# Optimization experiments

Hardware: AMD Instinct MI355X
Metric: run time of the kernel (lower is better)

The kernel has to match this reference:

```python
import jax, jax.numpy as jnp
import numpy as np

B, T, C, H = 8, 2048, 1024, 16
N_LAYER, LAYER_ID = 12, 1
NH = C // H           # head size = 64
CHUNK = 256


def setup_inputs() -> dict:
    key = jax.random.key(0)
    ks = jax.random.split(key, 10)
    # deterministic init matching the torch __init__
    ratio_0_to_1 = LAYER_ID / (N_LAYER - 1)
    ratio_1_to_almost0 = 1.0 - LAYER_ID / N_LAYER
    ddd = np.arange(C, dtype=np.float32) / C
    time_maa_k = (1.0 - ddd ** ratio_1_to_almost0).astype(np.float32)
    time_maa_v = (1.0 - (ddd ** ratio_1_to_almost0 + 0.3 * ratio_0_to_1)).astype(np.float32)
    time_maa_r = (1.0 - ddd ** (0.5 * ratio_1_to_almost0)).astype(np.float32)
    h_idx = np.arange(H, dtype=np.float32)
    time_decay = (-6.0 + 5.0 * (h_idx / (H - 1)) ** (0.7 + 1.3 * ratio_0_to_1)).astype(np.float32)
    s = 0.02
    return {
        "x": jax.random.normal(ks[0], (B, T, C), jnp.float32),
        "volatility": jax.random.uniform(ks[1], (B, T), jnp.float32),
        "Wvol": jax.random.normal(ks[2], (C, 1), jnp.float32) * s,
        "bvol": jnp.zeros((C,), jnp.float32),
        "time_maa_k": jnp.asarray(time_maa_k),
        "time_maa_v": jnp.asarray(time_maa_v),
        "time_maa_r": jnp.asarray(time_maa_r),
        "time_decay": jnp.asarray(time_decay),
        "Wk": jax.random.normal(ks[3], (C, C), jnp.float32) * s,
        "Wv": jax.random.normal(ks[4], (C, C), jnp.float32) * s,
        "Wr": jax.random.normal(ks[5], (C, C), jnp.float32) * s,
        "Wo": jax.random.normal(ks[6], (C, C), jnp.float32) * s,
        "gn_w": 1.0 + jax.random.normal(ks[7], (C,), jnp.float32) * s,
        "gn_b": jax.random.normal(ks[8], (C,), jnp.float32) * s,
    }


def reference(x, volatility, Wvol, bvol, time_maa_k, time_maa_v, time_maa_r,
              time_decay, Wk, Wv, Wr, Wo, gn_w, gn_b):
    b, t, c = x.shape
    h = time_decay.shape[0]
    n = c // h
    nc = t // CHUNK

    # volatility gating: sigmoid(Linear(1->C))
    v_emb = jax.nn.sigmoid(volatility[:, :, None] * Wvol[:, 0] + bvol)  # (B,T,C)
    x = x * v_emb

    # time shift (zero-pad one step at the front, drop last)
    xx = jnp.pad(x, ((0, 0), (1, 0), (0, 0)))[:, :-1] - x
    xk = x + xx * time_maa_k
    xv = x + xx * time_maa_v
    xr = x + xx * time_maa_r

    r = (xr @ Wr.T).reshape(b, t, h, n).transpose(0, 2, 1, 3)  # (B,H,T,N)
    k = (xk @ Wk.T).reshape(b, t, h, n).transpose(0, 2, 1, 3)
    v = (xv @ Wv.T).reshape(b, t, h, n).transpose(0, 2, 1, 3)

    w = jnp.exp(-jnp.exp(time_decay))[None, :, None, None]  # scalar decay per head

    # chunked linear-attention recurrence (faithful to torch loop, chunk=256, no intra-chunk mask)
    rc = r.reshape(b, h, nc, CHUNK, n).transpose(2, 0, 1, 3, 4)  # (nc,B,H,CK,N)
    kc = k.reshape(b, h, nc, CHUNK, n).transpose(2, 0, 1, 3, 4)
    vc = v.reshape(b, h, nc, CHUNK, n).transpose(2, 0, 1, 3, 4)

    def step(state, rkv):
        rr, kk, vv = rkv  # each (B,H,CK,N)
        att = jnp.einsum('bhtn,bhsn->bhts', rr, kk)            # r @ k^T
        y = w * (jnp.einsum('bhts,bhsn->bhtn', att, vv)
                 + jnp.einsum('bhtn,bhnm->bhtm', rr, state))
        new_state = w * (state + jnp.einsum('bhsn,bhsm->bhnm', kk, vv))
        return new_state, y

    state0 = jnp.zeros((b, h, n, n), x.dtype)
    _, ys = jax.lax.scan(step, state0, (rc, kc, vc))            # (nc,B,H,CK,N)
    y = ys.transpose(1, 2, 0, 3, 4).reshape(b, h, t, n)
    y = y.transpose(0, 2, 1, 3).reshape(b * t, c)

    # GroupNorm with H groups over channels
    yg = y.reshape(b * t, h, n)
    mu = yg.mean(-1, keepdims=True)
    var = yg.var(-1, keepdims=True)
    yg = (yg - mu) * jax.lax.rsqrt(var + 1e-5)
    y = (yg.reshape(b * t, c) * gn_w + gn_b).reshape(b, t, c)

    return y @ Wo.T  # dropout is identity in eval
```

## Files before the change

### kernel.cpp

```cpp
#include <hip/hip_runtime.h>

typedef unsigned short u16;
typedef __attribute__((ext_vector_type(4))) unsigned int u32x4;
typedef __attribute__((ext_vector_type(4))) float f32x4;
typedef __attribute__((ext_vector_type(8))) short s16x8;

#define B_ 8
#define T_ 2048
#define C_ 1024
#define H_ 16
#define HS_ 64
#define CHUNK_ 256
#define NC_ 8

union U8 { u32x4 u; u16 h[8]; };

__device__ __forceinline__ float b2f(u16 v) {
    union { unsigned int i; float f; } c; c.i = ((unsigned int)v) << 16; return c.f;
}
__device__ __forceinline__ u16 f2b(float f) {
    union { float f; unsigned int i; } c; c.f = f;
    unsigned int i = c.i;
    return (u16)((i + 0x7FFFu + ((i >> 16) & 1u)) >> 16);
}
__device__ __forceinline__ float fsig(float z) {
    return __builtin_amdgcn_rcpf(1.f + __expf(-z));
}

typedef __attribute__((address_space(1))) void GV;
typedef __attribute__((address_space(3))) void LV;
__device__ __forceinline__ void glds16(const void* g, void* l) {
    __builtin_amdgcn_global_load_lds((GV*)g, (LV*)l, 16, 0, 0);
}

__global__ __launch_bounds__(256) void cvt4_kernel(
    const float* __restrict__ s0, const float* __restrict__ s1,
    const float* __restrict__ s2, const float* __restrict__ s3,
    u16* __restrict__ dst)
{
    int i = blockIdx.x * 256 + threadIdx.x;
    int m = i >> 17;
    const float* s = (m == 0) ? s0 : (m == 1) ? s1 : (m == 2) ? s2 : s3;
    size_t j = (size_t)(i & 131071) * 8;
    f32x4 a = *reinterpret_cast<const f32x4*>(s + j);
    f32x4 b = *reinterpret_cast<const f32x4*>(s + j + 4);
    U8 o;
    #pragma unroll
    for (int k = 0; k < 4; k++) { o.h[k] = f2b(a[k]); o.h[4 + k] = f2b(b[k]); }
    *reinterpret_cast<u32x4*>(dst + (size_t)m * C_ * C_ + j) = o.u;
}

__global__ __launch_bounds__(256) void mix_kernel(
    const float* __restrict__ x, const float* __restrict__ vol,
    const float* __restrict__ Wvol, const float* __restrict__ bvol,
    const float* __restrict__ mk, const float* __restrict__ mv, const float* __restrict__ mr,
    u16* __restrict__ xk, u16* __restrict__ xv, u16* __restrict__ xr)
{
    int idx = blockIdx.x * 256 + threadIdx.x;
    int c0 = (idx & 127) * 8;
    int bt8 = idx >> 7;
    int t0  = (bt8 & 255) * 8;
    int b   = bt8 >> 8;
    size_t rowOff = ((size_t)b * T_ + t0) * C_ + c0;

    float wv[8], bv[8], mkv[8], mvv[8], mrv[8];
    #pragma unroll
    for (int j = 0; j < 8; j += 4) {
        f32x4 a;
        a = *reinterpret_cast<const f32x4*>(Wvol + c0 + j);
        wv[j] = a[0]; wv[j+1] = a[1]; wv[j+2] = a[2]; wv[j+3] = a[3];
        a = *reinterpret_cast<const f32x4*>(bvol + c0 + j);
        bv[j] = a[0]; bv[j+1] = a[1]; bv[j+2] = a[2]; bv[j+3] = a[3];
        a = *reinterpret_cast<const f32x4*>(mk + c0 + j);
        mkv[j] = a[0]; mkv[j+1] = a[1]; mkv[j+2] = a[2]; mkv[j+3] = a[3];
        a = *reinterpret_cast<const f32x4*>(mv + c0 + j);
        mvv[j] = a[0]; mvv[j+1] = a[1]; mvv[j+2] = a[2]; mvv[j+3] = a[3];
        a = *reinterpret_cast<const f32x4*>(mr + c0 + j);
        mrv[j] = a[0]; mrv[j+1] = a[1]; mrv[j+2] = a[2]; mrv[j+3] = a[3];
    }

    const float* volb = vol + (size_t)b * T_;
    float gp[8];
    if (t0 == 0) {
        #pragma unroll
        for (int j = 0; j < 8; j++) gp[j] = 0.f;
    } else {
        float vp = volb[t0 - 1];
        #pragma unroll
        for (int j = 0; j < 8; j += 4) {
            f32x4 a = *reinterpret_cast<const f32x4*>(x + rowOff - C_ + j);
            gp[j]   = a[0] * fsig(vp * wv[j]   + bv[j]);
            gp[j+1] = a[1] * fsig(vp * wv[j+1] + bv[j+1]);
            gp[j+2] = a[2] * fsig(vp * wv[j+2] + bv[j+2]);
            gp[j+3] = a[3] * fsig(vp * wv[j+3] + bv[j+3]);
        }
    }

    #pragma unroll
    for (int s = 0; s < 8; s++) {
        float vc = volb[t0 + s];
        size_t off = rowOff + (size_t)s * C_;
        float g[8];
        #pragma unroll
        for (int j = 0; j < 8; j += 4) {
            f32x4 a = *reinterpret_cast<const f32x4*>(x + off + j);
            g[j]   = a[0] * fsig(vc * wv[j]   + bv[j]);
            g[j+1] = a[1] * fsig(vc * wv[j+1] + bv[j+1]);
            g[j+2] = a[2] * fsig(vc * wv[j+2] + bv[j+2]);
            g[j+3] = a[3] * fsig(vc * wv[j+3] + bv[j+3]);
        }
        U8 ok, ov, orr;
        #pragma unroll
        for (int j = 0; j < 8; j++) {
            float xx = gp[j] - g[j];
            ok.h[j]  = f2b(g[j] + xx * mkv[j]);
            ov.h[j]  = f2b(g[j] + xx * mvv[j]);
            orr.h[j] = f2b(g[j] + xx * mrv[j]);
            gp[j] = g[j];
        }
        *reinterpret_cast<u32x4*>(xk + off) = ok.u;
        *reinterpret_cast<u32x4*>(xv + off) = ov.u;
        *reinterpret_cast<u32x4*>(xr + off) = orr.u;
    }
}

#define GBM_ 256
#define GBN_ 256
#define GBK_ 64
#define GK_  1024
#define GNT_ 16
#define GEMM_LDS_BYTES 131072

template<int MODE>
__global__ __launch_bounds__(512, 2) void gemm_bt(
    const u16* __restrict__ A, const u16* __restrict__ W, void* __restrict__ Cc)
{
    extern __shared__ __align__(16) u16 lds[];
    const int tid  = threadIdx.x;
    const int lane = tid & 63, w = tid >> 6;
    const int r16  = lane & 15, quad = lane >> 4;
    const int wm2  = w >> 2;
    const int wn4  = w & 3;
    const int id   = blockIdx.x;
    const int bm   = id & 63, bn = id >> 6;

    const u16* Ab = A + (size_t)bm * GBM_ * GK_;
    const u16* Wb = W + (size_t)bn * GBN_ * GK_;

    const int srow8  = lane >> 3;
    const int schunk = ((lane & 7) ^ srow8) * 8;
    const u16* aSrc = Ab + (size_t)(w * 16 + srow8) * GK_ + schunk;
    const u16* bSrc = Wb + (size_t)(w * 16 + srow8) * GK_ + schunk;

    const int fA0 = (wm2 * 128 + r16) * 64;
    const int fB0 = 16384 + (wn4 * 64 + r16) * 64;
    const int c0 = ((quad)     ^ (r16 & 7)) * 8;
    const int c1 = ((quad | 4) ^ (r16 & 7)) * 8;

    f32x4 acc[8][4];
    #pragma unroll
    for (int mi = 0; mi < 8; mi++)
        #pragma unroll
        for (int ni = 0; ni < 4; ni++)
            acc[mi][ni] = f32x4{0.f, 0.f, 0.f, 0.f};

#define STQ(tt, h) do {                                                       \
    const size_t ko_ = (size_t)(tt) * 64;                                     \
    u16* db_ = lds + (((tt) & 1) * 32768) + ((h) * 128 + w * 16) * 64;        \
    glds16(aSrc + (size_t)((h) * 128)     * GK_ + ko_, db_);                  \
    glds16(aSrc + (size_t)((h) * 128 + 8) * GK_ + ko_, db_ + 512);            \
    glds16(bSrc + (size_t)((h) * 128)     * GK_ + ko_, db_ + 16384);          \
    glds16(bSrc + (size_t)((h) * 128 + 8) * GK_ + ko_, db_ + 16384 + 512);    \
} while (0)

#define PH_BAR() do { asm volatile("" ::: "memory");                          \
    __builtin_amdgcn_s_barrier(); asm volatile("" ::: "memory"); } while (0)
#define PH_LGKM0() do { asm volatile("s_waitcnt lgkmcnt(0)" ::: "memory");    \
    __builtin_amdgcn_sched_barrier(0); } while (0)
#define LDFA(CO) { _Pragma("unroll") for (int mi = 0; mi < 8; mi++)           \
    fa[mi] = *reinterpret_cast<const s16x8*>(lds + pb + fA0 + mi * 1024 + (CO)); }
#define LDFB(NH, CO) { _Pragma("unroll") for (int ni = 0; ni < 2; ni++)       \
    fb[ni] = *reinterpret_cast<const s16x8*>(lds + pb + fB0 + ((NH) * 2 + ni) * 1024 + (CO)); }
#define MFMA16(NH) do { __builtin_amdgcn_s_setprio(1);                        \
    _Pragma("unroll") for (int mi = 0; mi < 8; mi++) {                        \
        acc[mi][(NH)*2+0] = __builtin_amdgcn_mfma_f32_16x16x32_bf16(          \
            fa[mi], fb[0], acc[mi][(NH)*2+0], 0, 0, 0);                       \
        acc[mi][(NH)*2+1] = __builtin_amdgcn_mfma_f32_16x16x32_bf16(          \
            fa[mi], fb[1], acc[mi][(NH)*2+1], 0, 0, 0);                       \
    } __builtin_amdgcn_s_setprio(0); } while (0)

    STQ(0, 0);
    STQ(0, 1);
    asm volatile("s_waitcnt vmcnt(0)" ::: "memory");
    PH_BAR();

    for (int t = 0; t < GNT_; ++t) {
        const int pb = (t & 1) * 32768;
        s16x8 fa[8], fb[2];
        LDFA(c0); LDFB(0, c0);
        if (t + 1 < GNT_) STQ(t + 1, 0);
        PH_BAR(); PH_LGKM0(); MFMA16(0); PH_BAR();
        LDFB(1, c0);
        PH_BAR(); PH_LGKM0(); MFMA16(1); PH_BAR();
        LDFA(c1); LDFB(0, c1);
        if (t + 1 < GNT_) STQ(t + 1, 1);
        PH_BAR(); PH_LGKM0(); MFMA16(0); PH_BAR();
        LDFB(1, c1);
        PH_BAR(); PH_LGKM0(); MFMA16(1);
        asm volatile("s_waitcnt vmcnt(0)" ::: "memory");
        PH_BAR();
    }
#undef STQ
#undef LDFA
#undef LDFB
#undef MFMA16
#undef PH_LGKM0
#undef PH_BAR

    if constexpr (MODE == 0) {
        float* C = (float*)Cc;
        #pragma unroll
        for (int mi = 0; mi < 8; mi++) {
            int row0 = bm * GBM_ + wm2 * 128 + mi * 16 + quad * 4;
            #pragma unroll
            for (int ni = 0; ni < 4; ni++) {
                int col = bn * GBN_ + wn4 * 64 + ni * 16 + r16;
                #pragma unroll
                for (int i = 0; i < 4; i++)
                    C[(size_t)(row0 + i) * C_ + col] = acc[mi][ni][i];
            }
        }
    } else if constexpr (MODE == 1) {
        u16* ep = lds + w * 4608;
        u16* C = (u16*)Cc;
        #pragma unroll
        for (int half = 0; half < 2; half++) {
            #pragma unroll
            for (int mi2 = 0; mi2 < 4; mi2++) {
                int mi = half * 4 + mi2;
                #pragma unroll
                for (int ni = 0; ni < 4; ni++)
                    #pragma unroll
                    for (int i = 0; i < 4; i++)
                        ep[(mi2 * 16 + quad * 4 + i) * 72 + ni * 16 + r16] =
                            f2b(acc[mi][ni][i]);
            }
            asm volatile("s_waitcnt lgkmcnt(0)" ::: "memory");
            __builtin_amdgcn_sched_barrier(0);
            #pragma unroll
            for (int it = 0; it < 8; it++) {
                int rr = it * 8 + (lane >> 3);
                u32x4 val = *reinterpret_cast<const u32x4*>(ep + rr * 72 + (lane & 7) * 8);
                size_t grow = (size_t)(bm * GBM_ + wm2 * 128 + half * 64 + rr);
                *reinterpret_cast<u32x4*>(
                    C + grow * C_ + bn * GBN_ + wn4 * 64 + (lane & 7) * 8) = val;
            }
            asm volatile("s_waitcnt vmcnt(0) lgkmcnt(0)" ::: "memory");
        }
    } else {
        u16* ep = lds + w * 8192;
        #pragma unroll
        for (int mi = 0; mi < 8; mi++) {
            const int chunk = mi * 2 + (quad >> 1);
            const int rsub = (quad & 1) * 4;
            #pragma unroll
            for (int ni = 0; ni < 4; ni++) {
                const int col = ni * 16 + r16;
                u16* p = ep + col * 128 + ((chunk ^ col) & 15) * 8 + rsub;
                p[0] = f2b(acc[mi][ni][0]);
                p[1] = f2b(acc[mi][ni][1]);
                p[2] = f2b(acc[mi][ni][2]);
                p[3] = f2b(acc[mi][ni][3]);
            }
        }
        asm volatile("s_waitcnt lgkmcnt(0)" ::: "memory");
        __builtin_amdgcn_sched_barrier(0);
        u16* C = (u16*)Cc;
        const int cl = lane >> 2, ch4 = lane & 3;
        #pragma unroll
        for (int it = 0; it < 16; it++) {
            const int col_l = (it & 3) * 16 + cl;
            const int chunk = (it >> 2) * 4 + ch4;
            u32x4 val = *reinterpret_cast<const u32x4*>(
                ep + col_l * 128 + ((chunk ^ col_l) & 15) * 8);
            const size_t gcol = (size_t)(bn * GBN_ + wn4 * 64 + col_l);
            const size_t grow = (size_t)(bm * GBM_ + wm2 * 128 + chunk * 8);
            *reinterpret_cast<u32x4*>(C + gcol * 16384 + grow) = val;
        }
    }
}

__global__ __launch_bounds__(256) void kvscan_kernel(
    const u16* __restrict__ kT, const u16* __restrict__ vT,
    const float* __restrict__ td, u16* __restrict__ stT)
{
    const int bm2 = blockIdx.x;
    const int mh = bm2 & 1, bh = bm2 >> 1;
    const int h = bh & (H_ - 1), b = bh >> 4;
    const float wdec = expf(-expf(td[h]));
    const int tid = threadIdx.x, lane = tid & 63, wave = tid >> 6;
    const int r16 = lane & 15, quad = lane >> 4;
    const int n0 = wave * 16;

    const size_t tb = (size_t)b * T_ + quad * 8;
    const u16* vr  = vT + (size_t)(h * HS_ + n0 + r16) * 16384 + tb;
    const u16* kr0 = kT + (size_t)(h * HS_ + mh * 32 + r16) * 16384 + tb;
    const u16* kr1 = kr0 + (size_t)16 * 16384;

    f32x4 st[2];
    st[0] = f32x4{0.f, 0.f, 0.f, 0.f};
    st[1] = f32x4{0.f, 0.f, 0.f, 0.f};

    for (int j = 0; j < NC_; j++) {
        f32x4 acc[2];
        acc[0] = f32x4{0.f, 0.f, 0.f, 0.f};
        acc[1] = f32x4{0.f, 0.f, 0.f, 0.f};
        const int jb = j * CHUNK_;
        #pragma unroll
        for (int ks = 0; ks < 8; ks++) {
            const int co = jb + ks * 32;
            s16x8 fa  = *reinterpret_cast<const s16x8*>(vr  + co);
            s16x8 fb0 = *reinterpret_cast<const s16x8*>(kr0 + co);
            s16x8 fb1 = *reinterpret_cast<const s16x8*>(kr1 + co);
            acc[0] = __builtin_amdgcn_mfma_f32_16x16x32_bf16(fa, fb0, acc[0], 0, 0, 0);
            acc[1] = __builtin_amdgcn_mfma_f32_16x16x32_bf16(fa, fb1, acc[1], 0, 0, 0);
        }
        u16* out = stT + ((size_t)bh * NC_ + j) * 4096;
        #pragma unroll
        for (int mi = 0; mi < 2; mi++) {
            st[mi] = (st[mi] + acc[mi]) * wdec;
            #pragma unroll
            for (int i = 0; i < 4; i++)
                out[(n0 + quad * 4 + i) * HS_ + mh * 32 + mi * 16 + r16] =
                    f2b(st[mi][i]);
        }
    }
}

__global__ __launch_bounds__(256) void rstate_gn_kernel(
    const u16* __restrict__ r, const u16* __restrict__ stT,
    const float* __restrict__ gnw, const float* __restrict__ gnb, u16* __restrict__ ygn)
{
    int blk = blockIdx.x;
    int c  = blk & (NC_ - 1);
    int bh = blk >> 3;
    int h = bh & (H_ - 1);
    int b = bh >> 4;
    __shared__ __align__(16) u16 sT[HS_ * 72];
    int tid = threadIdx.x, lane = tid & 63, wave = tid >> 6;
    int r16 = lane & 15, quad = lane >> 4;

    const u16* sg = stT + (size_t)blk * (HS_ * HS_);
    for (int i = tid; i < 512; i += 256) {
        int n = i >> 3, c8 = (i & 7) * 8;
        *reinterpret_cast<u32x4*>(&sT[n * 72 + c8]) =
            *reinterpret_cast<const u32x4*>(sg + n * HS_ + c8);
    }
    __syncthreads();

    size_t rowBase = (size_t)(b * T_ + c * CHUNK_ + wave * 64);
    f32x4 acc[4][4];
    #pragma unroll
    for (int mi = 0; mi < 4; mi++)
        #pragma unroll
        for (int ni = 0; ni < 4; ni++)
            acc[mi][ni] = f32x4{0.f, 0.f, 0.f, 0.f};

    #pragma unroll
    for (int ks = 0; ks < 2; ks++) {
        int kb = ks * 32 + quad * 8;
        s16x8 fa[4], fb[4];
        #pragma unroll
        for (int mi = 0; mi < 4; mi++)
            fa[mi] = *reinterpret_cast<const s16x8*>(
                r + (rowBase + mi * 16 + r16) * C_ + h * HS_ + kb);
        #pragma unroll
        for (int ni = 0; ni < 4; ni++)
            fb[ni] = *reinterpret_cast<const s16x8*>(&sT[(ni * 16 + r16) * 72 + kb]);
        #pragma unroll
        for (int mi = 0; mi < 4; mi++)
            #pragma unroll
            for (int ni = 0; ni < 4; ni++)
                acc[mi][ni] = __builtin_amdgcn_mfma_f32_16x16x32_bf16(fa[mi], fb[ni], acc[mi][ni], 0, 0, 0);
    }

    float gwv[4], gbv[4];
    #pragma unroll
    for (int ni = 0; ni < 4; ni++) {
        int col = ni * 16 + r16;
        gwv[ni] = gnw[h * HS_ + col];
        gbv[ni] = gnb[h * HS_ + col];
    }
    #pragma unroll
    for (int mi = 0; mi < 4; mi++) {
        float s1[4], s2[4];
        #pragma unroll
        for (int i = 0; i < 4; i++) {
            float s = 0.f, ss = 0.f;
            #pragma unroll
            for (int ni = 0; ni < 4; ni++) {
                float v = acc[mi][ni][i];
                s += v; ss += v * v;
            }
            s1[i] = s; s2[i] = ss;
        }
        #pragma unroll
        for (int d = 1; d < 16; d <<= 1) {
            #pragma unroll
            for (int i = 0; i < 4; i++) {
                s1[i] += __shfl_xor(s1[i], d);
                s2[i] += __shfl_xor(s2[i], d);
            }
        }
        #pragma unroll
        for (int i = 0; i < 4; i++) {
            float mu = s1[i] * (1.f / 64.f);
            float var = s2[i] * (1.f / 64.f) - mu * mu;
            float sc = rsqrtf(var + 1e-5f);
            size_t ob = (rowBase + mi * 16 + quad * 4 + i) * C_ + h * HS_;
            #pragma unroll
            for (int ni = 0; ni < 4; ni++)
                ygn[ob + ni * 16 + r16] = f2b((acc[mi][ni][i] - mu) * sc * gwv[ni] + gbv[ni]);
        }
    }
}

extern "C" void kernel_launch(void* const* d_in, const int* in_sizes, int n_in,
                              void* d_out, int out_size, void* d_ws, size_t ws_size,
                              hipStream_t stream) {
    const float* x    = (const float*)d_in[0];
    const float* vol  = (const float*)d_in[1];
    const float* Wvol = (const float*)d_in[2];
    const float* bvol = (const float*)d_in[3];
    const float* mk   = (const float*)d_in[4];
    const float* mv   = (const float*)d_in[5];
    const float* mr   = (const float*)d_in[6];
    const float* td   = (const float*)d_in[7];
    const float* Wk   = (const float*)d_in[8];
    const float* Wv   = (const float*)d_in[9];
    const float* Wr   = (const float*)d_in[10];
    const float* Wo   = (const float*)d_in[11];
    const float* gnw  = (const float*)d_in[12];
    const float* gnb  = (const float*)d_in[13];
    float* out = (float*)d_out;

    static bool init_attr = []() {
        hipFuncSetAttribute(reinterpret_cast<const void*>(gemm_bt<0>),
                            hipFuncAttributeMaxDynamicSharedMemorySize, GEMM_LDS_BYTES);
        hipFuncSetAttribute(reinterpret_cast<const void*>(gemm_bt<1>),
                            hipFuncAttributeMaxDynamicSharedMemorySize, GEMM_LDS_BYTES);
        hipFuncSetAttribute(reinterpret_cast<const void*>(gemm_bt<2>),
                            hipFuncAttributeMaxDynamicSharedMemorySize, GEMM_LDS_BYTES);
        return true;
    }();
    (void)init_attr;

    char* ws = (char*)d_ws;
    const size_t SLOT = (size_t)B_ * T_ * C_ * 2;
    u16* xr = (u16*)(ws + 0 * SLOT);
    u16* xk = (u16*)(ws + 1 * SLOT);
    u16* xv = (u16*)(ws + 2 * SLOT);
    u16* rb = (u16*)(ws + 3 * SLOT);
    u16* kbT = (u16*)(ws + 0 * SLOT);
    u16* vbT = (u16*)(ws + 1 * SLOT);
    u16* stT = (u16*)(ws + 2 * SLOT + SLOT / 2);
    u16* ygn = (u16*)(ws + 0 * SLOT);
    u16* wtb = (u16*)(ws + 4 * SLOT);
    u16* wrb = wtb;
    u16* wkb = wrb + (size_t)C_ * C_;
    u16* wvb = wkb + (size_t)C_ * C_;
    u16* wob = wvb + (size_t)C_ * C_;

    cvt4_kernel<<<dim3(4 * (C_ * C_ / 8) / 256), dim3(256), 0, stream>>>(Wr, Wk, Wv, Wo, wtb);

    mix_kernel<<<dim3(1024), dim3(256), 0, stream>>>(
        x, vol, Wvol, bvol, mk, mv, mr, xk, xv, xr);

    gemm_bt<1><<<dim3(256), dim3(512), GEMM_LDS_BYTES, stream>>>(xr, wrb, rb);
    gemm_bt<2><<<dim3(256), dim3(512), GEMM_LDS_BYTES, stream>>>(xk, wkb, kbT);
    gemm_bt<2><<<dim3(256), dim3(512), GEMM_LDS_BYTES, stream>>>(xv, wvb, vbT);

    kvscan_kernel<<<dim3(B_ * H_ * 2), dim3(256), 0, stream>>>(kbT, vbT, td, stT);

    rstate_gn_kernel<<<dim3(B_ * H_ * NC_), dim3(256), 0, stream>>>(rb, stT, gnw, gnb, ygn);

    gemm_bt<0><<<dim3(256), dim3(512), GEMM_LDS_BYTES, stream>>>(ygn, wob, out);
}
```

Baseline: 339.4 us.

## Tile transposed K/V layout and stage kvscan loads through LDS with wider blocks

The MODE-2 GEMM epilogue now writes K^T/V^T in 16x32 tiles (16 channels by 32 timesteps, each tile contiguous) instead of plain row-major transposed rows. kvscan uses 512 threads and double-buffered global-to-LDS staging of those tiles, and each of its 8 waves computes one 16x16 state block. Separately, mix_kernel handles 4 timesteps per thread with twice as many blocks, and the GEMM issues both next-tile stage loads at the start of each iteration. The aim is coalesced, overlapped memory access in the scan and more parallelism, in exchange for 96KB of LDS per block and coupling the tiled layout between the two kernels.

```diff
diff --git a/kernel.cpp b/kernel.cpp
--- a/kernel.cpp
+++ b/kernel.cpp
@@ -58,9 +58,9 @@
 {
     int idx = blockIdx.x * 256 + threadIdx.x;
     int c0 = (idx & 127) * 8;
-    int bt8 = idx >> 7;
-    int t0  = (bt8 & 255) * 8;
-    int b   = bt8 >> 8;
+    int bt4 = idx >> 7;
+    int t0  = (bt4 & 511) * 4;
+    int b   = bt4 >> 9;
     size_t rowOff = ((size_t)b * T_ + t0) * C_ + c0;
 
     float wv[8], bv[8], mkv[8], mvv[8], mrv[8];
@@ -97,7 +97,7 @@
     }
 
     #pragma unroll
-    for (int s = 0; s < 8; s++) {
+    for (int s = 0; s < 4; s++) {
         float vc = volb[t0 + s];
         size_t off = rowOff + (size_t)s * C_;
         float g[8];
@@ -198,12 +198,11 @@
         const int pb = (t & 1) * 32768;
         s16x8 fa[8], fb[2];
         LDFA(c0); LDFB(0, c0);
-        if (t + 1 < GNT_) STQ(t + 1, 0);
+        if (t + 1 < GNT_) { STQ(t + 1, 0); STQ(t + 1, 1); }
         PH_BAR(); PH_LGKM0(); MFMA16(0); PH_BAR();
         LDFB(1, c0);
         PH_BAR(); PH_LGKM0(); MFMA16(1); PH_BAR();
         LDFA(c1); LDFB(0, c1);
-        if (t + 1 < GNT_) STQ(t + 1, 1);
         PH_BAR(); PH_LGKM0(); MFMA16(0); PH_BAR();
         LDFB(1, c1);
         PH_BAR(); PH_LGKM0(); MFMA16(1);
@@ -277,64 +276,79 @@
         __builtin_amdgcn_sched_barrier(0);
         u16* C = (u16*)Cc;
         const int cl = lane >> 2, ch4 = lane & 3;
+        const int gc0 = bn * 16 + wn4 * 4;
+        const int tt0 = bm * 8 + wm2 * 4;
         #pragma unroll
         for (int it = 0; it < 16; it++) {
             const int col_l = (it & 3) * 16 + cl;
             const int chunk = (it >> 2) * 4 + ch4;
             u32x4 val = *reinterpret_cast<const u32x4*>(
                 ep + col_l * 128 + ((chunk ^ col_l) & 15) * 8);
-            const size_t gcol = (size_t)(bn * GBN_ + wn4 * 64 + col_l);
-            const size_t grow = (size_t)(bm * GBM_ + wm2 * 128 + chunk * 8);
-            *reinterpret_cast<u32x4*>(C + gcol * 16384 + grow) = val;
-        }
-    }
-}
-
-__global__ __launch_bounds__(256) void kvscan_kernel(
+            const size_t tile = (size_t)(gc0 + (it & 3)) * 512 + tt0 + (it >> 2);
+            *reinterpret_cast<u32x4*>(C + tile * 512 + cl * 32 + ch4 * 8) = val;
+        }
+    }
+}
+
+#define KVS_LDS_BYTES 98304
+
+__global__ __launch_bounds__(512) void kvscan_kernel(
     const u16* __restrict__ kT, const u16* __restrict__ vT,
     const float* __restrict__ td, u16* __restrict__ stT)
 {
+    extern __shared__ __align__(16) u16 klds[];
     const int bm2 = blockIdx.x;
     const int mh = bm2 & 1, bh = bm2 >> 1;
     const int h = bh & (H_ - 1), b = bh >> 4;
     const float wdec = expf(-expf(td[h]));
-    const int tid = threadIdx.x, lane = tid & 63, wave = tid >> 6;
+    const int tid = threadIdx.x, lane = tid & 63, w = tid >> 6;
     const int r16 = lane & 15, quad = lane >> 4;
-    const int n0 = wave * 16;
-
-    const size_t tb = (size_t)b * T_ + quad * 8;
-    const u16* vr  = vT + (size_t)(h * HS_ + n0 + r16) * 16384 + tb;
-    const u16* kr0 = kT + (size_t)(h * HS_ + mh * 32 + r16) * 16384 + tb;
-    const u16* kr1 = kr0 + (size_t)16 * 16384;
-
-    f32x4 st[2];
-    st[0] = f32x4{0.f, 0.f, 0.f, 0.f};
-    st[1] = f32x4{0.f, 0.f, 0.f, 0.f};
-
-    for (int j = 0; j < NC_; j++) {
-        f32x4 acc[2];
-        acc[0] = f32x4{0.f, 0.f, 0.f, 0.f};
-        acc[1] = f32x4{0.f, 0.f, 0.f, 0.f};
-        const int jb = j * CHUNK_;
+    const int cgn = w >> 1;
+    const int ck  = w & 1;
+    const int tt0 = b * 64;
+    const int loff = r16 * 32 + quad * 8;
+
+#define KSTG(jj, bb) do {                                                     \
+    u16* db_ = klds + (bb) * 24576;                                           \
+    _Pragma("unroll")                                                         \
+    for (int q = 0; q < 6; q++) {                                             \
+        const int tau = w * 6 + q;                                            \
+        const u16* src;                                                       \
+        if (tau < 32)                                                         \
+            src = vT + ((size_t)(h * 4 + (tau >> 3)) * 512 +                  \
+                        tt0 + (jj) * 8 + (tau & 7)) * 512;                    \
+        else                                                                  \
+            src = kT + ((size_t)(h * 4 + mh * 2 + ((tau - 32) >> 3)) * 512 +  \
+                        tt0 + (jj) * 8 + ((tau - 32) & 7)) * 512;             \
+        glds16(src + (size_t)lane * 8, db_ + tau * 512);                      \
+    }                                                                         \
+} while (0)
+
+    KSTG(0, 0);
+
+    f32x4 st = f32x4{0.f, 0.f, 0.f, 0.f};
+    for (int j = 0; j < NC_; ++j) {
+        asm volatile("s_waitcnt vmcnt(0)" ::: "memory");
+        __syncthreads();
+        if (j + 1 < NC_) KSTG(j + 1, (j + 1) & 1);
+        const u16* bb = klds + (j & 1) * 24576;
+        f32x4 acc = f32x4{0.f, 0.f, 0.f, 0.f};
         #pragma unroll
         for (int ks = 0; ks < 8; ks++) {
-            const int co = jb + ks * 32;
-            s16x8 fa  = *reinterpret_cast<const s16x8*>(vr  + co);
-            s16x8 fb0 = *reinterpret_cast<const s16x8*>(kr0 + co);
-            s16x8 fb1 = *reinterpret_cast<const s16x8*>(kr1 + co);
-            acc[0] = __builtin_amdgcn_mfma_f32_16x16x32_bf16(fa, fb0, acc[0], 0, 0, 0);
-            acc[1] = __builtin_amdgcn_mfma_f32_16x16x32_bf16(fa, fb1, acc[1], 0, 0, 0);
-        }
+            s16x8 fa = *reinterpret_cast<const s16x8*>(
+                bb + (cgn * 8 + ks) * 512 + loff);
+            s16x8 fb = *reinterpret_cast<const s16x8*>(
+                bb + (32 + ck * 8 + ks) * 512 + loff);
+            acc = __builtin_amdgcn_mfma_f32_16x16x32_bf16(fa, fb, acc, 0, 0, 0);
+        }
+        st = (st + acc) * wdec;
         u16* out = stT + ((size_t)bh * NC_ + j) * 4096;
         #pragma unroll
-        for (int mi = 0; mi < 2; mi++) {
-            st[mi] = (st[mi] + acc[mi]) * wdec;
-            #pragma unroll
-            for (int i = 0; i < 4; i++)
-                out[(n0 + quad * 4 + i) * HS_ + mh * 32 + mi * 16 + r16] =
-                    f2b(st[mi][i]);
-        }
-    }
+        for (int i = 0; i < 4; i++)
+            out[(cgn * 16 + quad * 4 + i) * HS_ + mh * 32 + ck * 16 + r16] =
+                f2b(st[i]);
+    }
+#undef KSTG
 }
 
 __global__ __launch_bounds__(256) void rstate_gn_kernel(
@@ -451,6 +465,8 @@
                             hipFuncAttributeMaxDynamicSharedMemorySize, GEMM_LDS_BYTES);
         hipFuncSetAttribute(reinterpret_cast<const void*>(gemm_bt<2>),
                             hipFuncAttributeMaxDynamicSharedMemorySize, GEMM_LDS_BYTES);
+        hipFuncSetAttribute(reinterpret_cast<const void*>(kvscan_kernel),
+                            hipFuncAttributeMaxDynamicSharedMemorySize, KVS_LDS_BYTES);
         return true;
     }();
     (void)init_attr;
@@ -473,14 +489,14 @@
 
     cvt4_kernel<<<dim3(4 * (C_ * C_ / 8) / 256), dim3(256), 0, stream>>>(Wr, Wk, Wv, Wo, wtb);
 
-    mix_kernel<<<dim3(1024), dim3(256), 0, stream>>>(
+    mix_kernel<<<dim3(2048), dim3(256), 0, stream>>>(
         x, vol, Wvol, bvol, mk, mv, mr, xk, xv, xr);
 
     gemm_bt<1><<<dim3(256), dim3(512), GEMM_LDS_BYTES, stream>>>(xr, wrb, rb);
     gemm_bt<2><<<dim3(256), dim3(512), GEMM_LDS_BYTES, stream>>>(xk, wkb, kbT);
     gemm_bt<2><<<dim3(256), dim3(512), GEMM_LDS_BYTES, stream>>>(xv, wvb, vbT);
 
-    kvscan_kernel<<<dim3(B_ * H_ * 2), dim3(256), 0, stream>>>(kbT, vbT, td, stT);
+    kvscan_kernel<<<dim3(B_ * H_ * 2), dim3(512), KVS_LDS_BYTES, stream>>>(kbT, vbT, td, stT);
 
     rstate_gn_kernel<<<dim3(B_ * H_ * NC_), dim3(256), 0, stream>>>(rb, stT, gnw, gnb, ygn);
 
```

New measurement: 346.0 us. Within noise of the previous version (+1.9%).
